# Optimization experiments

Measured on AMD Instinct MI355X. Metric: run time of the kernel, lower is better.

## Reference

```python
import jax, jax.numpy as jnp
import numpy as np

N_NODES = 100000
N_EDGES = 1600000
IN_FEATS = 128
HEADS = 4
OUT_FEATS = 32
NEG_SLOPE = 0.2


def setup_inputs() -> dict:
    key = jax.random.key(0)
    k1, k2, k3, k4, k5, k6 = jax.random.split(key, 6)
    feat = jax.random.normal(k1, (N_NODES, IN_FEATS), dtype=jnp.float32)
    # nn.Linear(in_feats, out_feats*num_heads).weight -> [H*D_out, D_in]
    W = jax.random.normal(k2, (HEADS * OUT_FEATS, IN_FEATS), dtype=jnp.float32) * (1.0 / np.sqrt(IN_FEATS))
    attn_l = jax.random.normal(k3, (1, HEADS, OUT_FEATS), dtype=jnp.float32) * 0.1
    attn_r = jax.random.normal(k4, (1, HEADS, OUT_FEATS), dtype=jnp.float32) * 0.1
    src = jax.random.randint(k5, (N_EDGES,), 0, N_NODES, dtype=jnp.int32)
    dst = jax.random.randint(k6, (N_EDGES,), 0, N_NODES, dtype=jnp.int32)
    return {"feat": feat, "W": W, "attn_l": attn_l, "attn_r": attn_r, "src": src, "dst": dst}


def reference(feat, W, attn_l, attn_r, src, dst):
    N = feat.shape[0]
    H, D = attn_l.shape[1], attn_l.shape[2]
    # fc: feat @ W.T -> [N, H, D]
    ft = (feat @ W.T).reshape(N, H, D)
    el = jnp.sum(ft * attn_l, axis=-1)  # [N, H]
    er = jnp.sum(ft * attn_r, axis=-1)  # [N, H]
    # SDDMM edge scores (u_add_v) + leaky relu
    e = el[src] + er[dst]  # [E, H]
    e = jnp.where(e > 0, e, NEG_SLOPE * e)
    # segment softmax over edges grouped by destination node
    emax = jax.ops.segment_max(e, dst, num_segments=N)  # [N, H]
    ez = jnp.exp(e - emax[dst])
    esum = jax.ops.segment_sum(ez, dst, num_segments=N)  # [N, H]
    a = ez / esum[dst]  # [E, H]
    # weighted SpMM aggregation (u_mul_e + sum by dst)
    out = jax.ops.segment_sum(ft[src] * a[:, :, None], dst, num_segments=N)  # [N, H, D]
    return out
```

## Files before the change

kernel.cpp:

```cpp
#include <hip/hip_runtime.h>
#include <hip/hip_fp16.h>

#define IN_FEATS 128
#define HEADS 4
#define D_OUT 32
#define HD 128
#define NEG_SLOPE 0.2f

#define BSHIFT 6
#define BSIZE 64
#define CAP 1280
#define NBMAX 1600

typedef _Float16 half8 __attribute__((ext_vector_type(8)));
typedef _Float16 half4v __attribute__((ext_vector_type(4)));
typedef float floatx4 __attribute__((ext_vector_type(4)));

#define LSTR 40
#define OSTR 136

__global__ __launch_bounds__(256) void gemm_ft(const float* __restrict__ feat,
                                               const float* __restrict__ W,
                                               const float* __restrict__ al,
                                               const float* __restrict__ ar,
                                               __half* __restrict__ ft_h,
                                               float* __restrict__ el,
                                               float* __restrict__ er,
                                               int* __restrict__ bcursor,
                                               int N, int NB) {
    __shared__ __align__(16) _Float16 sh[128 * OSTR];
    _Float16* Als = sh;
    _Float16* Wls = sh + 5120;
    const int t = threadIdx.x;
    const int w = t >> 6, lane = t & 63, quad = lane >> 4, l15 = lane & 15;
    const int nodeBase = blockIdx.x * 128;

    if (blockIdx.x == 0)
        for (int b = t; b < NB; b += 256) bcursor[b] = b * CAP;

    floatx4 acc[2][8] = {};

    for (int kk = 0; kk < 4; ++kk) {
        const int k0 = kk * 32;
#pragma unroll
        for (int i = 0; i < 4; ++i) {
            int idx = i * 256 + t;
            int row = idx >> 3;
            int q = idx & 7;
            int node = nodeBase + row;
            float4 v = make_float4(0.f, 0.f, 0.f, 0.f);
            if (node < N) v = *(const float4*)(feat + (size_t)node * IN_FEATS + k0 + q * 4);
            half4v hv = {(_Float16)v.x, (_Float16)v.y, (_Float16)v.z, (_Float16)v.w};
            *(half4v*)&Als[row * LSTR + q * 4] = hv;
            float4 wv = *(const float4*)(W + (size_t)row * IN_FEATS + k0 + q * 4);
            half4v hw = {(_Float16)wv.x, (_Float16)wv.y, (_Float16)wv.z, (_Float16)wv.w};
            *(half4v*)&Wls[row * LSTR + q * 4] = hw;
        }
        __syncthreads();
        half8 af0 = *(half8*)&Als[(w * 32 + l15) * LSTR + quad * 8];
        half8 af1 = *(half8*)&Als[(w * 32 + 16 + l15) * LSTR + quad * 8];
        half8 bf[8];
#pragma unroll
        for (int nt = 0; nt < 8; ++nt)
            bf[nt] = *(half8*)&Wls[(nt * 16 + l15) * LSTR + quad * 8];
#pragma unroll
        for (int nt = 0; nt < 8; ++nt) {
            acc[0][nt] = __builtin_amdgcn_mfma_f32_16x16x32_f16(af0, bf[nt], acc[0][nt], 0, 0, 0);
            acc[1][nt] = __builtin_amdgcn_mfma_f32_16x16x32_f16(af1, bf[nt], acc[1][nt], 0, 0, 0);
        }
        __syncthreads();
    }

#pragma unroll
    for (int mt = 0; mt < 2; ++mt)
#pragma unroll
        for (int nt = 0; nt < 8; ++nt)
#pragma unroll
            for (int r = 0; r < 4; ++r)
                sh[(w * 32 + mt * 16 + quad * 4 + r) * OSTR + nt * 16 + l15] =
                    (_Float16)acc[mt][nt][r];
    __syncthreads();

    const int row = t >> 1, seg = t & 1;
    const int node = nodeBase + row;
    half8 hv[8];
#pragma unroll
    for (int j = 0; j < 8; ++j) hv[j] = *(half8*)&sh[row * OSTR + seg * 64 + j * 8];

    float accl0 = 0.f, accl1 = 0.f, accr0 = 0.f, accr1 = 0.f;
#pragma unroll
    for (int j = 0; j < 8; ++j) {
        float4 a0 = *(const float4*)(al + seg * 64 + j * 8);
        float4 a1 = *(const float4*)(al + seg * 64 + j * 8 + 4);
        float4 r0 = *(const float4*)(ar + seg * 64 + j * 8);
        float4 r1 = *(const float4*)(ar + seg * 64 + j * 8 + 4);
        float v0 = (float)hv[j][0], v1 = (float)hv[j][1], v2 = (float)hv[j][2], v3 = (float)hv[j][3];
        float v4 = (float)hv[j][4], v5 = (float)hv[j][5], v6 = (float)hv[j][6], v7 = (float)hv[j][7];
        float dl = v0 * a0.x + v1 * a0.y + v2 * a0.z + v3 * a0.w
                 + v4 * a1.x + v5 * a1.y + v6 * a1.z + v7 * a1.w;
        float dr = v0 * r0.x + v1 * r0.y + v2 * r0.z + v3 * r0.w
                 + v4 * r1.x + v5 * r1.y + v6 * r1.z + v7 * r1.w;
        if (j < 4) { accl0 += dl; accr0 += dr; }
        else       { accl1 += dl; accr1 += dr; }
    }
    if (node < N) {
#pragma unroll
        for (int j = 0; j < 8; ++j)
            *(half8*)(ft_h + (size_t)node * HD + seg * 64 + j * 8) = hv[j];
        el[node * 4 + seg * 2 + 0] = accl0;
        el[node * 4 + seg * 2 + 1] = accl1;
        er[node * 4 + seg * 2 + 0] = accr0;
        er[node * 4 + seg * 2 + 1] = accr1;
    }
}

#define MAXCHUNK 3200

__global__ __launch_bounds__(256) void bin_scatter(const int* __restrict__ src,
                                                   const int* __restrict__ dst,
                                                   int* __restrict__ bcursor,
                                                   int* __restrict__ bedge,
                                                   int E, int NB, int chunk) {
    __shared__ int recL[MAXCHUNK];
    __shared__ unsigned short bL[MAXCHUNK];
    __shared__ int cnt[NBMAX];
    __shared__ int base[NBMAX];
    int t = threadIdx.x;
    int e0 = blockIdx.x * chunk;
    if (e0 >= E) return;
    int e1 = e0 + chunk; if (e1 > E) e1 = E;
    int ne = e1 - e0;
    for (int b = t; b < NB; b += 256) cnt[b] = 0;
    __syncthreads();
    for (int i = t; i < ne; i += 256) {
        int d = dst[e0 + i];
        int s = src[e0 + i];
        int b = d >> BSHIFT;
        recL[i] = s | ((d & (BSIZE - 1)) << 17);
        bL[i] = (unsigned short)b;
        atomicAdd(&cnt[b], 1);
    }
    __syncthreads();
    for (int b = t; b < NB; b += 256) {
        int c = cnt[b];
        base[b] = c ? atomicAdd(&bcursor[b], c) : 0;
    }
    __syncthreads();
    for (int b = t; b < NB; b += 256) cnt[b] = 0;
    __syncthreads();
    for (int i = t; i < ne; i += 256) {
        int b = bL[i];
        int p = base[b] + atomicAdd(&cnt[b], 1);
        if (p < (b + 1) * CAP)
            bedge[p] = recL[i];
    }
}

__global__ __launch_bounds__(256) void bucket_aggregate(const __half* __restrict__ ft_h,
                                                        const float* __restrict__ el,
                                                        const float* __restrict__ er,
                                                        const int* __restrict__ bcursor,
                                                        const int* __restrict__ bedge,
                                                        float* __restrict__ out, int N) {
    __shared__ int eS[CAP];
    __shared__ uint2 eW[CAP];
    __shared__ float4 er4L[BSIZE];
    __shared__ int cnt[BSIZE];
    __shared__ int exs[BSIZE];
    __shared__ int pos[BSIZE];
    const int b = blockIdx.x, t = threadIdx.x;
    const int s0 = b * CAP;
    const int node0 = b << BSHIFT;
    int cntE = bcursor[b] - s0;
    if (cntE > CAP) cntE = CAP;
    if (t < BSIZE) {
        cnt[t] = 0;
        int n = node0 + t;
        er4L[t] = (n < N) ? *(const float4*)(er + (size_t)n * 4)
                          : make_float4(0.f, 0.f, 0.f, 0.f);
    }
    __syncthreads();
    for (int i = t; i < cntE; i += 256)
        atomicAdd(&cnt[bedge[s0 + i] >> 17], 1);
    __syncthreads();
    if (t < BSIZE) {
        int x = cnt[t];
        int inc = x;
#pragma unroll
        for (int off = 1; off < 64; off <<= 1) {
            int y = __shfl_up(inc, off);
            if (t >= off) inc += y;
        }
        exs[t] = inc - x;
        pos[t] = inc - x;
    }
    __syncthreads();
    for (int i = t; i < cntE; i += 256) {
        int v = bedge[s0 + i];
        int dl = v >> 17;
        int s = v & 0x1FFFF;
        float4 el4 = *(const float4*)(el + (size_t)s * 4);
        float4 e4 = er4L[dl];
        float x0 = el4.x + e4.x; x0 = x0 > 0.f ? x0 : NEG_SLOPE * x0;
        float x1 = el4.y + e4.y; x1 = x1 > 0.f ? x1 : NEG_SLOPE * x1;
        float x2 = el4.z + e4.z; x2 = x2 > 0.f ? x2 : NEG_SLOPE * x2;
        float x3 = el4.w + e4.w; x3 = x3 > 0.f ? x3 : NEG_SLOPE * x3;
        __half2 p01 = __floats2half2_rn(__expf(x0), __expf(x1));
        __half2 p23 = __floats2half2_rn(__expf(x2), __expf(x3));
        uint2 pk;
        pk.x = *(unsigned int*)&p01;
        pk.y = *(unsigned int*)&p23;
        int p = atomicAdd(&pos[dl], 1);
        eS[p] = s;
        eW[p] = pk;
    }
    __syncthreads();

    const int wid = t >> 6, lane = t & 63;
    const int g = lane >> 4;
    const int q = lane & 15;
    const int h = q >> 2;
    const unsigned short* eWu = (const unsigned short*)eW;

    for (int dl = wid; dl < BSIZE; dl += 4) {
        int n = node0 + dl;
        if (n >= N) break;
        int start = exs[dl];
        int end = start + cnt[dl];

        float a0 = 0.f, a1 = 0.f, a2 = 0.f, a3 = 0.f;
        float a4 = 0.f, a5 = 0.f, a6 = 0.f, a7 = 0.f;
        float ws = 0.f;

        int e = start + g;
        int s = (e < end) ? eS[e] : 0;
        int4 raw = make_int4(0, 0, 0, 0);
        if (e < end) raw = *(const int4*)(ft_h + (size_t)s * HD + q * 8);

        while (e < end) {
            int en = e + 4;
            int sn = (en < end) ? eS[en] : 0;
            int4 rawn = make_int4(0, 0, 0, 0);
            if (en < end) rawn = *(const int4*)(ft_h + (size_t)sn * HD + q * 8);

            unsigned short us = eWu[e * 4 + h];
            float w = __half2float(*(__half*)&us);
            float2 f0 = __half22float2(*(__half2*)&raw.x);
            float2 f1 = __half22float2(*(__half2*)&raw.y);
            float2 f2 = __half22float2(*(__half2*)&raw.z);
            float2 f3 = __half22float2(*(__half2*)&raw.w);
            a0 += w * f0.x; a1 += w * f0.y;
            a2 += w * f1.x; a3 += w * f1.y;
            a4 += w * f2.x; a5 += w * f2.y;
            a6 += w * f3.x; a7 += w * f3.y;
            ws += w;

            e = en; s = sn; raw = rawn;
        }
        a0 += __shfl_xor(a0, 16); a0 += __shfl_xor(a0, 32);
        a1 += __shfl_xor(a1, 16); a1 += __shfl_xor(a1, 32);
        a2 += __shfl_xor(a2, 16); a2 += __shfl_xor(a2, 32);
        a3 += __shfl_xor(a3, 16); a3 += __shfl_xor(a3, 32);
        a4 += __shfl_xor(a4, 16); a4 += __shfl_xor(a4, 32);
        a5 += __shfl_xor(a5, 16); a5 += __shfl_xor(a5, 32);
        a6 += __shfl_xor(a6, 16); a6 += __shfl_xor(a6, 32);
        a7 += __shfl_xor(a7, 16); a7 += __shfl_xor(a7, 32);
        ws += __shfl_xor(ws, 16); ws += __shfl_xor(ws, 32);
        float inv = ws > 0.f ? 1.0f / ws : 0.f;
        float r0 = (g == 0 ? a0 : g == 1 ? a2 : g == 2 ? a4 : a6) * inv;
        float r1 = (g == 0 ? a1 : g == 1 ? a3 : g == 2 ? a5 : a7) * inv;
        *(float2*)(out + (size_t)n * HD + q * 8 + g * 2) = make_float2(r0, r1);
    }
}

extern "C" void kernel_launch(void* const* d_in, const int* in_sizes, int n_in,
                              void* d_out, int out_size, void* d_ws, size_t ws_size,
                              hipStream_t stream) {
    const float* feat = (const float*)d_in[0];
    const float* W    = (const float*)d_in[1];
    const float* al   = (const float*)d_in[2];
    const float* ar   = (const float*)d_in[3];
    const int* src    = (const int*)d_in[4];
    const int* dst    = (const int*)d_in[5];
    float* out        = (float*)d_out;

    const int N = in_sizes[0] / IN_FEATS;
    const int E = in_sizes[4];
    const int NB = (N + BSIZE - 1) >> BSHIFT;

    char* ws = (char*)d_ws;
    size_t off = 0;
    auto alloc = [&](size_t bytes) {
        void* p = ws + off;
        off += (bytes + 255) & ~(size_t)255;
        return p;
    };
    __half* ft_h   = (__half*)alloc((size_t)N * HD * 2);
    float* el      = (float*)alloc((size_t)N * 4 * 4);
    float* er      = (float*)alloc((size_t)N * 4 * 4);
    int*   bcursor = (int*)alloc((size_t)NBMAX * 4);
    int*   bedge   = (int*)alloc((size_t)NB * CAP * 4);
    (void)ws_size;

    gemm_ft<<<(N + 127) / 128, 256, 0, stream>>>(feat, W, al, ar, ft_h, el, er, bcursor, N, NB);
    int grid2 = 512;
    int chunk = (E + grid2 - 1) / grid2;
    if (chunk > MAXCHUNK) chunk = MAXCHUNK;
    int nblk = (E + chunk - 1) / chunk;
    bin_scatter<<<nblk, 256, 0, stream>>>(src, dst, bcursor, bedge, E, NB, chunk);
    bucket_aggregate<<<NB, 256, 0, stream>>>(ft_h, el, er, bcursor, bedge, out, N);
}
```

Baseline: 246.4 us.

## Fuse GEMM and edge binning into one launch, unroll aggregate loop by two

The GEMM and edge bin-scatter kernels are merged into one grid. Leading blocks run the GEMM and trailing blocks bin edges, so the two independent stages can overlap on the GPU. The cursor init moves into a small separate kernel. The binning path now re-reads src/dst from global instead of staging records in shared memory, which keeps the shared footprint within the GEMM's allocation. The aggregation inner loop is changed from a software-prefetched one-edge-per-iteration loop to two edges per iteration, with both gathers issued together for more memory-level parallelism.

```diff
diff --git a/kernel.cpp b/kernel.cpp
--- a/kernel.cpp
+++ b/kernel.cpp
@@ -18,25 +18,66 @@
 
 #define LSTR 40
 #define OSTR 136
-
-__global__ __launch_bounds__(256) void gemm_ft(const float* __restrict__ feat,
-                                               const float* __restrict__ W,
-                                               const float* __restrict__ al,
-                                               const float* __restrict__ ar,
-                                               __half* __restrict__ ft_h,
-                                               float* __restrict__ el,
-                                               float* __restrict__ er,
-                                               int* __restrict__ bcursor,
-                                               int N, int NB) {
-    __shared__ __align__(16) _Float16 sh[128 * OSTR];
+#define SMEM_BYTES (128 * OSTR * 2)
+
+#define MAXCHUNK 3200
+
+__global__ void init_cursor(int* __restrict__ bcursor, int NB) {
+    int b = blockIdx.x * blockDim.x + threadIdx.x;
+    if (b < NB) bcursor[b] = b * CAP;
+}
+
+__global__ __launch_bounds__(256) void mega(const float* __restrict__ feat,
+                                            const float* __restrict__ W,
+                                            const float* __restrict__ al,
+                                            const float* __restrict__ ar,
+                                            const int* __restrict__ src,
+                                            const int* __restrict__ dst,
+                                            __half* __restrict__ ft_h,
+                                            float* __restrict__ el,
+                                            float* __restrict__ er,
+                                            int* __restrict__ bcursor,
+                                            int* __restrict__ bedge,
+                                            int N, int E, int NB,
+                                            int gemmBlocks, int chunk) {
+    __shared__ __align__(16) char smem[SMEM_BYTES];
+    const int t = threadIdx.x;
+
+    if (blockIdx.x >= gemmBlocks) {
+        int* cnt = (int*)smem;
+        int* base = cnt + NBMAX;
+        int bid = blockIdx.x - gemmBlocks;
+        int e0 = bid * chunk;
+        if (e0 >= E) return;
+        int e1 = e0 + chunk; if (e1 > E) e1 = E;
+        int ne = e1 - e0;
+        for (int b = t; b < NB; b += 256) cnt[b] = 0;
+        __syncthreads();
+        for (int i = t; i < ne; i += 256)
+            atomicAdd(&cnt[dst[e0 + i] >> BSHIFT], 1);
+        __syncthreads();
+        for (int b = t; b < NB; b += 256) {
+            int c = cnt[b];
+            base[b] = c ? atomicAdd(&bcursor[b], c) : 0;
+        }
+        __syncthreads();
+        for (int b = t; b < NB; b += 256) cnt[b] = 0;
+        __syncthreads();
+        for (int i = t; i < ne; i += 256) {
+            int d = dst[e0 + i];
+            int b = d >> BSHIFT;
+            int p = base[b] + atomicAdd(&cnt[b], 1);
+            if (p < (b + 1) * CAP)
+                bedge[p] = src[e0 + i] | ((d & (BSIZE - 1)) << 17);
+        }
+        return;
+    }
+
+    _Float16* sh = (_Float16*)smem;
     _Float16* Als = sh;
     _Float16* Wls = sh + 5120;
-    const int t = threadIdx.x;
     const int w = t >> 6, lane = t & 63, quad = lane >> 4, l15 = lane & 15;
     const int nodeBase = blockIdx.x * 128;
-
-    if (blockIdx.x == 0)
-        for (int b = t; b < NB; b += 256) bcursor[b] = b * CAP;
 
     floatx4 acc[2][8] = {};
 
@@ -111,48 +152,6 @@
         el[node * 4 + seg * 2 + 1] = accl1;
         er[node * 4 + seg * 2 + 0] = accr0;
         er[node * 4 + seg * 2 + 1] = accr1;
-    }
-}
-
-#define MAXCHUNK 3200
-
-__global__ __launch_bounds__(256) void bin_scatter(const int* __restrict__ src,
-                                                   const int* __restrict__ dst,
-                                                   int* __restrict__ bcursor,
-                                                   int* __restrict__ bedge,
-                                                   int E, int NB, int chunk) {
-    __shared__ int recL[MAXCHUNK];
-    __shared__ unsigned short bL[MAXCHUNK];
-    __shared__ int cnt[NBMAX];
-    __shared__ int base[NBMAX];
-    int t = threadIdx.x;
-    int e0 = blockIdx.x * chunk;
-    if (e0 >= E) return;
-    int e1 = e0 + chunk; if (e1 > E) e1 = E;
-    int ne = e1 - e0;
-    for (int b = t; b < NB; b += 256) cnt[b] = 0;
-    __syncthreads();
-    for (int i = t; i < ne; i += 256) {
-        int d = dst[e0 + i];
-        int s = src[e0 + i];
-        int b = d >> BSHIFT;
-        recL[i] = s | ((d & (BSIZE - 1)) << 17);
-        bL[i] = (unsigned short)b;
-        atomicAdd(&cnt[b], 1);
-    }
-    __syncthreads();
-    for (int b = t; b < NB; b += 256) {
-        int c = cnt[b];
-        base[b] = c ? atomicAdd(&bcursor[b], c) : 0;
-    }
-    __syncthreads();
-    for (int b = t; b < NB; b += 256) cnt[b] = 0;
-    __syncthreads();
-    for (int i = t; i < ne; i += 256) {
-        int b = bL[i];
-        int p = base[b] + atomicAdd(&cnt[b], 1);
-        if (p < (b + 1) * CAP)
-            bedge[p] = recL[i];
     }
 }
 
@@ -232,30 +231,31 @@
         float a4 = 0.f, a5 = 0.f, a6 = 0.f, a7 = 0.f;
         float ws = 0.f;
 
-        int e = start + g;
-        int s = (e < end) ? eS[e] : 0;
-        int4 raw = make_int4(0, 0, 0, 0);
-        if (e < end) raw = *(const int4*)(ft_h + (size_t)s * HD + q * 8);
-
-        while (e < end) {
-            int en = e + 4;
-            int sn = (en < end) ? eS[en] : 0;
-            int4 rawn = make_int4(0, 0, 0, 0);
-            if (en < end) rawn = *(const int4*)(ft_h + (size_t)sn * HD + q * 8);
-
-            unsigned short us = eWu[e * 4 + h];
-            float w = __half2float(*(__half*)&us);
-            float2 f0 = __half22float2(*(__half2*)&raw.x);
-            float2 f1 = __half22float2(*(__half2*)&raw.y);
-            float2 f2 = __half22float2(*(__half2*)&raw.z);
-            float2 f3 = __half22float2(*(__half2*)&raw.w);
-            a0 += w * f0.x; a1 += w * f0.y;
-            a2 += w * f1.x; a3 += w * f1.y;
-            a4 += w * f2.x; a5 += w * f2.y;
-            a6 += w * f3.x; a7 += w * f3.y;
-            ws += w;
-
-            e = en; s = sn; raw = rawn;
+        for (int bb = start; bb < end; bb += 8) {
+            int e0 = bb + g;
+            int e1 = e0 + 4;
+            bool v0 = e0 < end, v1 = e1 < end;
+            int sA = v0 ? eS[e0] : 0;
+            int sB = v1 ? eS[e1] : 0;
+            unsigned short uA = v0 ? eWu[e0 * 4 + h] : (unsigned short)0;
+            unsigned short uB = v1 ? eWu[e1 * 4 + h] : (unsigned short)0;
+            int4 rawA = *(const int4*)(ft_h + (size_t)sA * HD + q * 8);
+            int4 rawB = *(const int4*)(ft_h + (size_t)sB * HD + q * 8);
+            float w0 = v0 ? __half2float(*(__half*)&uA) : 0.f;
+            float w1 = v1 ? __half2float(*(__half*)&uB) : 0.f;
+            float2 fA0 = __half22float2(*(__half2*)&rawA.x);
+            float2 fA1 = __half22float2(*(__half2*)&rawA.y);
+            float2 fA2 = __half22float2(*(__half2*)&rawA.z);
+            float2 fA3 = __half22float2(*(__half2*)&rawA.w);
+            float2 fB0 = __half22float2(*(__half2*)&rawB.x);
+            float2 fB1 = __half22float2(*(__half2*)&rawB.y);
+            float2 fB2 = __half22float2(*(__half2*)&rawB.z);
+            float2 fB3 = __half22float2(*(__half2*)&rawB.w);
+            a0 += w0 * fA0.x + w1 * fB0.x;  a1 += w0 * fA0.y + w1 * fB0.y;
+            a2 += w0 * fA1.x + w1 * fB1.x;  a3 += w0 * fA1.y + w1 * fB1.y;
+            a4 += w0 * fA2.x + w1 * fB2.x;  a5 += w0 * fA2.y + w1 * fB2.y;
+            a6 += w0 * fA3.x + w1 * fB3.x;  a7 += w0 * fA3.y + w1 * fB3.y;
+            ws += w0 + w1;
         }
         a0 += __shfl_xor(a0, 16); a0 += __shfl_xor(a0, 32);
         a1 += __shfl_xor(a1, 16); a1 += __shfl_xor(a1, 32);
@@ -302,11 +302,14 @@
     int*   bedge   = (int*)alloc((size_t)NB * CAP * 4);
     (void)ws_size;
 
-    gemm_ft<<<(N + 127) / 128, 256, 0, stream>>>(feat, W, al, ar, ft_h, el, er, bcursor, N, NB);
+    init_cursor<<<(NB + 255) / 256, 256, 0, stream>>>(bcursor, NB);
+    int gemmBlocks = (N + 127) / 128;
     int grid2 = 512;
     int chunk = (E + grid2 - 1) / grid2;
     if (chunk > MAXCHUNK) chunk = MAXCHUNK;
     int nblk = (E + chunk - 1) / chunk;
-    bin_scatter<<<nblk, 256, 0, stream>>>(src, dst, bcursor, bedge, E, NB, chunk);
+    mega<<<gemmBlocks + nblk, 256, 0, stream>>>(feat, W, al, ar, src, dst,
+                                                ft_h, el, er, bcursor, bedge,
+                                                N, E, NB, gemmBlocks, chunk);
     bucket_aggregate<<<NB, 256, 0, stream>>>(ft_h, el, er, bcursor, bedge, out, N);
 }
```

Result: no change. 245.0 us (-0.6%).
